# Kernel optimization log

Measured on AMD Instinct MI355X. Metric: run time of the kernel, lower is better.

The kernel has to match this reference:

```python
import jax, jax.numpy as jnp
import numpy as np

N = 100000      # nodes
E = 1600000     # directed edges (before self-loops)
F_IN, H1, H2 = 128, 64, 32


def setup_inputs() -> dict:
    key = jax.random.key(0)
    ks = jax.random.split(key, 8)
    x = jax.random.normal(ks[0], (N, F_IN), dtype=jnp.float32)
    edge_index = jax.random.randint(ks[1], (2, E), 0, N, dtype=jnp.int32)
    # GCNConv lin weights (no bias in lin; separate additive bias), glorot-ish scale
    W1 = jax.random.normal(ks[2], (F_IN, H1), dtype=jnp.float32) / np.sqrt(F_IN)
    b1 = jnp.zeros((H1,), dtype=jnp.float32)
    W2 = jax.random.normal(ks[3], (H1, H2), dtype=jnp.float32) / np.sqrt(H1)
    b2 = jnp.zeros((H2,), dtype=jnp.float32)
    Wfc = jax.random.normal(ks[4], (H2, 1), dtype=jnp.float32) / np.sqrt(H2)
    bfc = jnp.zeros((1,), dtype=jnp.float32)
    return {"x": x, "edge_index": edge_index, "W1": W1, "b1": b1,
            "W2": W2, "b2": b2, "Wfc": Wfc, "bfc": bfc}


def _gcn_norm(edge_index):
    # PyG GCNConv default: add self-loops, symmetric normalization D^-1/2 (A+I) D^-1/2
    loop = jnp.arange(N, dtype=edge_index.dtype)
    src = jnp.concatenate([edge_index[0], loop])
    dst = jnp.concatenate([edge_index[1], loop])
    deg = jax.ops.segment_sum(jnp.ones_like(dst, dtype=jnp.float32), dst, num_segments=N)
    dinv = jnp.where(deg > 0, jax.lax.rsqrt(deg), 0.0)
    norm = dinv[src] * dinv[dst]  # [E+N]
    return src, dst, norm


def _gcn_conv(x, W, b, src, dst, norm):
    h = x @ W                                 # project first (PyG order)
    msg = norm[:, None] * h[src]              # gather + scale
    agg = jax.ops.segment_sum(msg, dst, num_segments=N)  # scatter-add
    return agg + b


def reference(x, edge_index, W1, b1, W2, b2, Wfc, bfc):
    src, dst, norm = _gcn_norm(edge_index)
    h = jax.nn.relu(_gcn_conv(x, W1, b1, src, dst, norm))
    h = jax.nn.relu(_gcn_conv(h, W2, b2, src, dst, norm))
    return h @ Wfc + bfc
```

## Files before the change

### kernel.cpp

```cpp
#include <hip/hip_runtime.h>

#define N_NODES 100000
#define BSH 9
#define NBKT ((N_NODES + 511) >> BSH)
#define CH 7168
#define SLACK 10240

typedef unsigned int u32;
typedef unsigned short u16;
typedef unsigned char u8;
typedef __attribute__((ext_vector_type(8))) short s8v;
typedef __attribute__((ext_vector_type(4))) float f4v;

static __device__ __forceinline__ u16 f2bf(float f) {
    union { float f; u32 u; } c; c.f = f;
    u32 r = (c.u + 0x7fffu + ((c.u >> 16) & 1u)) >> 16;
    return (u16)r;
}
static __device__ __forceinline__ float bf2f_u(u16 h) {
    union { u32 u; float f; } c; c.u = ((u32)h) << 16;
    return c.f;
}
static __device__ __forceinline__ void acc2(u32 p, float& a, float& b) {
    union { u32 u; float f; } lo, hi;
    lo.u = p << 16;
    hi.u = p & 0xffff0000u;
    a += lo.f;
    b += hi.f;
}
static __device__ __forceinline__ void acc8(uint4 p, float* a) {
    acc2(p.x, a[0], a[1]); acc2(p.y, a[2], a[3]);
    acc2(p.z, a[4], a[5]); acc2(p.w, a[6], a[7]);
}


__global__ __launch_bounds__(256) void initcur_k(int* __restrict__ bcur) {
    bcur[threadIdx.x] = threadIdx.x * SLACK;
}

__global__ __launch_bounds__(256) void partition_k(const int* __restrict__ src,
        const int* __restrict__ dst, int* __restrict__ bcur,
        u32* __restrict__ bktBuf, int E, int TOT) {
    __shared__ int hist[256];
    __shared__ int lbase[256];
    __shared__ int gbase[256];
    __shared__ int ps[256];
    __shared__ u32 stage[CH];
    __shared__ u8 stageB[CH];
    int t = threadIdx.x;
    int base = blockIdx.x * CH;
    int cnt = min(CH, TOT - base);
    hist[t] = 0;
    __syncthreads();
    for (int i = t; i < cnt; i += 256) {
        int e = base + i;
        int d = (e < E) ? dst[e] : e - E;
        atomicAdd(&hist[d >> BSH], 1);
    }
    __syncthreads();
    ps[t] = hist[t];
    __syncthreads();
    for (int off = 1; off < 256; off <<= 1) {
        int val = ps[t];
        int add = (t >= off) ? ps[t - off] : 0;
        __syncthreads();
        ps[t] = val + add;
        __syncthreads();
    }
    lbase[t] = ps[t] - hist[t];
    gbase[t] = atomicAdd(&bcur[t], hist[t]);
    hist[t] = 0;
    __syncthreads();
    for (int i = t; i < cnt; i += 256) {
        int e = base + i;
        int s, d;
        if (e < E) { s = src[e]; d = dst[e]; }
        else       { s = d = e - E; }
        int b = d >> BSH;
        int lpos = lbase[b] + atomicAdd(&hist[b], 1);
        stage[lpos] = ((u32)(d & 511) << 17) | (u32)s;
        stageB[lpos] = (u8)b;
    }
    __syncthreads();
    for (int i = t; i < cnt; i += 256) {
        int b = stageB[i];
        bktBuf[gbase[b] + (i - lbase[b])] = stage[i];
    }
}

__global__ __launch_bounds__(256) void buildfill_k(const int* __restrict__ bcur,
        const u32* __restrict__ bktBuf, int* __restrict__ offsets,
        int* __restrict__ ends, float* __restrict__ dinv,
        int* __restrict__ srt_src) {
    __shared__ int hist[512];
    __shared__ int hscan[512];
    __shared__ int cur[512];
    __shared__ int ps[256];
    int t = threadIdx.x;
    int b = blockIdx.x;
    int v0 = b << BSH;
    int nv = min(512, N_NODES - v0);
    int base = b * SLACK;
    int cnt = bcur[b] - base;
    hist[t] = 0; hist[t + 256] = 0;
    cur[t] = 0;  cur[t + 256] = 0;
    __syncthreads();
    for (int i = t; i < cnt; i += 256)
        atomicAdd(&hist[bktBuf[base + i] >> 17], 1);
    __syncthreads();
    int a = hist[2 * t], bb = hist[2 * t + 1];
    int own = a + bb;
    ps[t] = own;
    __syncthreads();
    for (int off = 1; off < 256; off <<= 1) {
        int val = ps[t];
        int add = (t >= off) ? ps[t - off] : 0;
        __syncthreads();
        ps[t] = val + add;
        __syncthreads();
    }
    int excl2 = ps[t] - own;
    hscan[2 * t] = excl2;
    hscan[2 * t + 1] = excl2 + a;
    __syncthreads();
    for (int j = t; j < nv; j += 256) {
        int o = base + hscan[j];
        offsets[v0 + j] = o;
        ends[v0 + j] = o + hist[j];
        dinv[v0 + j] = rsqrtf((float)hist[j]);
    }
    for (int i = t; i < cnt; i += 256) {
        u32 it = bktBuf[base + i];
        int j = it >> 17;
        int pos = atomicAdd(&cur[j], 1);
        srt_src[base + hscan[j] + pos] = (int)(it & 0x1ffffu);
    }
}


static __device__ __forceinline__ void split8(const float* __restrict__ xp,
                                              s8v& hi, s8v& lo) {
    float4 v0 = *(const float4*)xp;
    float4 v1 = *(const float4*)(xp + 4);
    float xv[8] = {v0.x, v0.y, v0.z, v0.w, v1.x, v1.y, v1.z, v1.w};
#pragma unroll
    for (int j = 0; j < 8; ++j) {
        u16 h = f2bf(xv[j]);
        hi[j] = (short)h;
        lo[j] = (short)f2bf(xv[j] - bf2f_u(h));
    }
}

__global__ __launch_bounds__(256) void gemm1_k(const float* __restrict__ x,
                                               const float* __restrict__ W1,
                                               const float* __restrict__ dinv,
                                               u16* __restrict__ h1b) {
    __shared__ __attribute__((aligned(16))) short Bs[2][4][4][512];
    int t = threadIdx.x;
    for (int i = t; i < 128 * 64; i += 256) {
        int k = i >> 6, c = i & 63;
        float w = W1[i];
        u16 h = f2bf(w);
        u16 l = f2bf(w - bf2f_u(h));
        int ks = k >> 5, kg = (k >> 3) & 3, kk = k & 7;
        int ct = c >> 4, col = c & 15;
        int idx = (kg * 16 + col) * 8 + kk;
        Bs[0][ks][ct][idx] = (short)h;
        Bs[1][ks][ct][idx] = (short)l;
    }
    __syncthreads();

    int lane = t & 63;
    int rows0 = (blockIdx.x * 4 + (t >> 6)) * 32;
    if (rows0 >= N_NODES) return;

    f4v acc[2][4];
#pragma unroll
    for (int rt = 0; rt < 2; ++rt)
#pragma unroll
        for (int ct = 0; ct < 4; ++ct)
            acc[rt][ct] = (f4v){0.f, 0.f, 0.f, 0.f};

    int arow = lane & 15;
    int kgl = lane >> 4;
#pragma unroll
    for (int ks = 0; ks < 4; ++ks) {
        s8v bh[4], bl[4];
#pragma unroll
        for (int ct = 0; ct < 4; ++ct) {
            bh[ct] = *(const s8v*)&Bs[0][ks][ct][lane * 8];
            bl[ct] = *(const s8v*)&Bs[1][ks][ct][lane * 8];
        }
#pragma unroll
        for (int rt = 0; rt < 2; ++rt) {
            s8v ah, al;
            const float* xp = x + (size_t)(rows0 + rt * 16 + arow) * 128
                                + ks * 32 + kgl * 8;
            split8(xp, ah, al);
#pragma unroll
            for (int ct = 0; ct < 4; ++ct) {
                acc[rt][ct] = __builtin_amdgcn_mfma_f32_16x16x32_bf16(
                    ah, bh[ct], acc[rt][ct], 0, 0, 0);
                acc[rt][ct] = __builtin_amdgcn_mfma_f32_16x16x32_bf16(
                    ah, bl[ct], acc[rt][ct], 0, 0, 0);
                acc[rt][ct] = __builtin_amdgcn_mfma_f32_16x16x32_bf16(
                    al, bh[ct], acc[rt][ct], 0, 0, 0);
            }
        }
    }

#pragma unroll
    for (int rt = 0; rt < 2; ++rt) {
        int rbase = rows0 + rt * 16 + ((lane >> 4) << 2);
        float dv[4];
#pragma unroll
        for (int r = 0; r < 4; ++r) dv[r] = dinv[rbase + r];
#pragma unroll
        for (int ct = 0; ct < 4; ++ct) {
            int col = ct * 16 + (lane & 15);
#pragma unroll
            for (int r = 0; r < 4; ++r)
                h1b[(size_t)(rbase + r) * 64 + col] = f2bf(acc[rt][ct][r] * dv[r]);
        }
    }
}


__global__ __launch_bounds__(256) void layer2_k(const int* __restrict__ offsets,
        const int* __restrict__ ends, const int* __restrict__ srt_src,
        const float* __restrict__ dinv, const u16* __restrict__ h1b,
        const float* __restrict__ b1, const float* __restrict__ W2,
        u16* __restrict__ h2b) {
    __shared__ float W2s[64 * 32];
    __shared__ float b1s[64];
    for (int i = threadIdx.x; i < 64 * 32; i += 256) W2s[i] = W2[i];
    if (threadIdx.x < 64) b1s[threadIdx.x] = b1[threadIdx.x];
    __syncthreads();
    int lane = threadIdx.x & 63;
    int f = lane & 15, q = lane >> 4;
    int v0 = blockIdx.x * 8 + (threadIdx.x >> 6) * 2;
    int v1 = v0 + 1;
    int i0 = offsets[v0], e0 = ends[v0];
    int i1 = offsets[v1], e1 = ends[v1];
    const uint2* rows = (const uint2*)h1b;
    float a0 = 0.f, a1 = 0.f, a2 = 0.f, a3 = 0.f;
    float c0 = 0.f, c1 = 0.f, c2 = 0.f, c3 = 0.f;
    while (i0 + 8 <= e0 && i1 + 8 <= e1) {
        int sA = srt_src[i0 + q];
        int sB = srt_src[i0 + 4 + q];
        int sC = srt_src[i1 + q];
        int sD = srt_src[i1 + 4 + q];
        uint2 pA = rows[sA * 16 + f];
        uint2 pB = rows[sB * 16 + f];
        uint2 pC = rows[sC * 16 + f];
        uint2 pD = rows[sD * 16 + f];
        acc2(pA.x, a0, a1); acc2(pA.y, a2, a3);
        acc2(pB.x, a0, a1); acc2(pB.y, a2, a3);
        acc2(pC.x, c0, c1); acc2(pC.y, c2, c3);
        acc2(pD.x, c0, c1); acc2(pD.y, c2, c3);
        i0 += 8; i1 += 8;
    }
    for (; i0 + 8 <= e0; i0 += 8) {
        int sA = srt_src[i0 + q], sB = srt_src[i0 + 4 + q];
        uint2 pA = rows[sA * 16 + f], pB = rows[sB * 16 + f];
        acc2(pA.x, a0, a1); acc2(pA.y, a2, a3);
        acc2(pB.x, a0, a1); acc2(pB.y, a2, a3);
    }
    for (; i0 < e0; i0 += 4) {
        int j = i0 + q;
        if (j < e0) {
            int s = srt_src[j];
            uint2 p = rows[s * 16 + f];
            acc2(p.x, a0, a1); acc2(p.y, a2, a3);
        }
    }
    for (; i1 + 8 <= e1; i1 += 8) {
        int sA = srt_src[i1 + q], sB = srt_src[i1 + 4 + q];
        uint2 pA = rows[sA * 16 + f], pB = rows[sB * 16 + f];
        acc2(pA.x, c0, c1); acc2(pA.y, c2, c3);
        acc2(pB.x, c0, c1); acc2(pB.y, c2, c3);
    }
    for (; i1 < e1; i1 += 4) {
        int j = i1 + q;
        if (j < e1) {
            int s = srt_src[j];
            uint2 p = rows[s * 16 + f];
            acc2(p.x, c0, c1); acc2(p.y, c2, c3);
        }
    }
    a0 += __shfl_xor(a0, 16, 64); a0 += __shfl_xor(a0, 32, 64);
    a1 += __shfl_xor(a1, 16, 64); a1 += __shfl_xor(a1, 32, 64);
    a2 += __shfl_xor(a2, 16, 64); a2 += __shfl_xor(a2, 32, 64);
    a3 += __shfl_xor(a3, 16, 64); a3 += __shfl_xor(a3, 32, 64);
    c0 += __shfl_xor(c0, 16, 64); c0 += __shfl_xor(c0, 32, 64);
    c1 += __shfl_xor(c1, 16, 64); c1 += __shfl_xor(c1, 32, 64);
    c2 += __shfl_xor(c2, 16, 64); c2 += __shfl_xor(c2, 32, 64);
    c3 += __shfl_xor(c3, 16, 64); c3 += __shfl_xor(c3, 32, 64);
    bool lo = (lane < 32);
    float dv = lo ? dinv[v0] : dinv[v1];
    float t0 = lo ? a0 : c0;
    float t1 = lo ? a1 : c1;
    float t2 = lo ? a2 : c2;
    float t3 = lo ? a3 : c3;
    float r0 = fmaxf(fmaf(dv, t0, b1s[4 * f + 0]), 0.f);
    float r1 = fmaxf(fmaf(dv, t1, b1s[4 * f + 1]), 0.f);
    float r2 = fmaxf(fmaf(dv, t2, b1s[4 * f + 2]), 0.f);
    float r3 = fmaxf(fmaf(dv, t3, b1s[4 * f + 3]), 0.f);
    int c = lane & 31;
    float o = 0.f;
#pragma unroll
    for (int j2 = 0; j2 < 16; ++j2) {
        float R0 = __shfl(r0, j2, 16);
        float R1 = __shfl(r1, j2, 16);
        float R2 = __shfl(r2, j2, 16);
        float R3 = __shfl(r3, j2, 16);
        o = fmaf(R0, W2s[(4 * j2 + 0) * 32 + c], o);
        o = fmaf(R1, W2s[(4 * j2 + 1) * 32 + c], o);
        o = fmaf(R2, W2s[(4 * j2 + 2) * 32 + c], o);
        o = fmaf(R3, W2s[(4 * j2 + 3) * 32 + c], o);
    }
    int vst = lo ? v0 : v1;
    h2b[vst * 32 + c] = f2bf(dv * o);
}


#define GATH3(ii, A, B, C, D) { \
    int s_ = srt_src[(ii) + oc]; \
    uint2 p_ = rows[s_ * 8 + f]; \
    acc2(p_.x, A, B); acc2(p_.y, C, D); }

__global__ __launch_bounds__(256) void layer3_k(const int* __restrict__ offsets,
        const int* __restrict__ ends, const int* __restrict__ srt_src,
        const float* __restrict__ dinv, const u16* __restrict__ h2b,
        const float* __restrict__ b2, const float* __restrict__ Wfc,
        const float* __restrict__ bfc, float* __restrict__ out) {
    int lane = threadIdx.x & 63;
    int f = lane & 7, oc = lane >> 3;
    int vb = blockIdx.x * 16 + (threadIdx.x >> 6) * 4;
    int i0 = offsets[vb],     e0 = ends[vb];
    int i1 = offsets[vb + 1], e1 = ends[vb + 1];
    int i2 = offsets[vb + 2], e2 = ends[vb + 2];
    int i3 = offsets[vb + 3], e3 = ends[vb + 3];
    const uint2* rows = (const uint2*)h2b;
    float A0=0.f,A1=0.f,A2=0.f,A3=0.f, B0=0.f,B1=0.f,B2=0.f,B3=0.f;
    float C0=0.f,C1=0.f,C2=0.f,C3=0.f, D0=0.f,D1=0.f,D2=0.f,D3=0.f;
    while (i0 + 8 <= e0 && i1 + 8 <= e1 && i2 + 8 <= e2 && i3 + 8 <= e3) {
        GATH3(i0, A0, A1, A2, A3);
        GATH3(i1, B0, B1, B2, B3);
        GATH3(i2, C0, C1, C2, C3);
        GATH3(i3, D0, D1, D2, D3);
        i0 += 8; i1 += 8; i2 += 8; i3 += 8;
    }
    while (i0 + 8 <= e0) { GATH3(i0, A0, A1, A2, A3); i0 += 8; }
    if (i0 + oc < e0)    { GATH3(i0, A0, A1, A2, A3); }
    while (i1 + 8 <= e1) { GATH3(i1, B0, B1, B2, B3); i1 += 8; }
    if (i1 + oc < e1)    { GATH3(i1, B0, B1, B2, B3); }
    while (i2 + 8 <= e2) { GATH3(i2, C0, C1, C2, C3); i2 += 8; }
    if (i2 + oc < e2)    { GATH3(i2, C0, C1, C2, C3); }
    while (i3 + 8 <= e3) { GATH3(i3, D0, D1, D2, D3); i3 += 8; }
    if (i3 + oc < e3)    { GATH3(i3, D0, D1, D2, D3); }
#define RED3(X) X += __shfl_xor(X, 8, 64); X += __shfl_xor(X, 16, 64); X += __shfl_xor(X, 32, 64)
    RED3(A0); RED3(A1); RED3(A2); RED3(A3);
    RED3(B0); RED3(B1); RED3(B2); RED3(B3);
    RED3(C0); RED3(C1); RED3(C2); RED3(C3);
    RED3(D0); RED3(D1); RED3(D2); RED3(D3);
    float w0 = Wfc[4 * f + 0], w1 = Wfc[4 * f + 1];
    float w2 = Wfc[4 * f + 2], w3 = Wfc[4 * f + 3];
    float g0 = b2[4 * f + 0], g1 = b2[4 * f + 1];
    float g2 = b2[4 * f + 2], g3 = b2[4 * f + 3];
    float dv0 = dinv[vb], dv1 = dinv[vb + 1], dv2 = dinv[vb + 2], dv3 = dinv[vb + 3];
    float p0 = fmaxf(fmaf(dv0, A0, g0), 0.f) * w0 + fmaxf(fmaf(dv0, A1, g1), 0.f) * w1
             + fmaxf(fmaf(dv0, A2, g2), 0.f) * w2 + fmaxf(fmaf(dv0, A3, g3), 0.f) * w3;
    float p1 = fmaxf(fmaf(dv1, B0, g0), 0.f) * w0 + fmaxf(fmaf(dv1, B1, g1), 0.f) * w1
             + fmaxf(fmaf(dv1, B2, g2), 0.f) * w2 + fmaxf(fmaf(dv1, B3, g3), 0.f) * w3;
    float p2 = fmaxf(fmaf(dv2, C0, g0), 0.f) * w0 + fmaxf(fmaf(dv2, C1, g1), 0.f) * w1
             + fmaxf(fmaf(dv2, C2, g2), 0.f) * w2 + fmaxf(fmaf(dv2, C3, g3), 0.f) * w3;
    float p3 = fmaxf(fmaf(dv3, D0, g0), 0.f) * w0 + fmaxf(fmaf(dv3, D1, g1), 0.f) * w1
             + fmaxf(fmaf(dv3, D2, g2), 0.f) * w2 + fmaxf(fmaf(dv3, D3, g3), 0.f) * w3;
#define REDP(X) X += __shfl_xor(X, 1, 64); X += __shfl_xor(X, 2, 64); X += __shfl_xor(X, 4, 64)
    REDP(p0); REDP(p1); REDP(p2); REDP(p3);
    if (lane == 0) {
        float bb = bfc[0];
        out[vb + 0] = p0 + bb;
        out[vb + 1] = p1 + bb;
        out[vb + 2] = p2 + bb;
        out[vb + 3] = p3 + bb;
    }
}


extern "C" void kernel_launch(void* const* d_in, const int* in_sizes, int n_in,
                              void* d_out, int out_size, void* d_ws, size_t ws_size,
                              hipStream_t stream) {
    const float* x   = (const float*)d_in[0];
    const int*   ei  = (const int*)d_in[1];
    const float* W1  = (const float*)d_in[2];
    const float* b1  = (const float*)d_in[3];
    const float* W2  = (const float*)d_in[4];
    const float* b2  = (const float*)d_in[5];
    const float* Wfc = (const float*)d_in[6];
    const float* bfc = (const float*)d_in[7];
    float* out = (float*)d_out;

    const int E = in_sizes[1] / 2;
    const int TOT = E + N_NODES;
    const int* src = ei;
    const int* dst = ei + E;

    int*   bcur    = (int*)d_ws;
    int*   offsets = bcur + 256;
    int*   ends    = offsets + N_NODES;
    int*   srt_src = ends + N_NODES;
    u32*   bktBuf  = (u32*)(srt_src + NBKT * SLACK);
    float* dinv    = (float*)(bktBuf + NBKT * SLACK);
    u16*   h1b     = (u16*)(dinv + N_NODES);
    u16*   h2b     = h1b + (size_t)N_NODES * 64;

    const int NCH = (TOT + CH - 1) / CH;

    initcur_k<<<1, 256, 0, stream>>>(bcur);
    partition_k<<<NCH, 256, 0, stream>>>(src, dst, bcur, bktBuf, E, TOT);
    buildfill_k<<<NBKT, 256, 0, stream>>>(bcur, bktBuf, offsets, ends, dinv,
                                          srt_src);

    const int GB1 = (N_NODES / 32 + 3) / 4;
    gemm1_k<<<GB1, 256, 0, stream>>>(x, W1, dinv, h1b);

    layer2_k<<<N_NODES / 8, 256, 0, stream>>>(offsets, ends, srt_src, dinv, h1b,
                                              b1, W2, h2b);
    layer3_k<<<N_NODES / 16, 256, 0, stream>>>(offsets, ends, srt_src, dinv, h2b,
                                               b2, Wfc, bfc, out);
}
```

Measured before the change: 187.7 us.

## Widen gathers to 16-byte rows and walk contiguous CSR span across owned nodes

Layers 2 and 3 now load 8 bf16 features per lane with uint4 gathers instead of 4 via uint2. Each wave walks the contiguous edge range covering all the nodes it owns, so a group that straddles a node boundary is split by the per-edge index rather than handled by a separate tail loop per node. The intent is fewer, wider memory transactions and fewer partially filled tail iterations. In exchange it adds more accumulator registers, longer shuffle reductions, and relies on the nodes' edge ranges being adjacent (ends[v0] == offsets[v1]); acc8 is assumed to be defined in the unseen part of the file.

```diff
diff --git a/kernel.cpp b/kernel.cpp
--- a/kernel.cpp
+++ b/kernel.cpp
@@ -237,97 +237,76 @@
     if (threadIdx.x < 64) b1s[threadIdx.x] = b1[threadIdx.x];
     __syncthreads();
     int lane = threadIdx.x & 63;
-    int f = lane & 15, q = lane >> 4;
+    int f = lane & 7, q = lane >> 3;
     int v0 = blockIdx.x * 8 + (threadIdx.x >> 6) * 2;
     int v1 = v0 + 1;
-    int i0 = offsets[v0], e0 = ends[v0];
-    int i1 = offsets[v1], e1 = ends[v1];
-    const uint2* rows = (const uint2*)h1b;
-    float a0 = 0.f, a1 = 0.f, a2 = 0.f, a3 = 0.f;
-    float c0 = 0.f, c1 = 0.f, c2 = 0.f, c3 = 0.f;
-    while (i0 + 8 <= e0 && i1 + 8 <= e1) {
-        int sA = srt_src[i0 + q];
-        int sB = srt_src[i0 + 4 + q];
-        int sC = srt_src[i1 + q];
-        int sD = srt_src[i1 + 4 + q];
-        uint2 pA = rows[sA * 16 + f];
-        uint2 pB = rows[sB * 16 + f];
-        uint2 pC = rows[sC * 16 + f];
-        uint2 pD = rows[sD * 16 + f];
-        acc2(pA.x, a0, a1); acc2(pA.y, a2, a3);
-        acc2(pB.x, a0, a1); acc2(pB.y, a2, a3);
-        acc2(pC.x, c0, c1); acc2(pC.y, c2, c3);
-        acc2(pD.x, c0, c1); acc2(pD.y, c2, c3);
-        i0 += 8; i1 += 8;
-    }
-    for (; i0 + 8 <= e0; i0 += 8) {
-        int sA = srt_src[i0 + q], sB = srt_src[i0 + 4 + q];
-        uint2 pA = rows[sA * 16 + f], pB = rows[sB * 16 + f];
-        acc2(pA.x, a0, a1); acc2(pA.y, a2, a3);
-        acc2(pB.x, a0, a1); acc2(pB.y, a2, a3);
-    }
-    for (; i0 < e0; i0 += 4) {
-        int j = i0 + q;
-        if (j < e0) {
-            int s = srt_src[j];
-            uint2 p = rows[s * 16 + f];
-            acc2(p.x, a0, a1); acc2(p.y, a2, a3);
+    int beg = offsets[v0], m = ends[v0], end = ends[v1];
+    const uint4* rows = (const uint4*)h1b;
+    float a[8] = {0.f,0.f,0.f,0.f,0.f,0.f,0.f,0.f};
+    float c[8] = {0.f,0.f,0.f,0.f,0.f,0.f,0.f,0.f};
+    int i = beg;
+    for (; i + 16 <= m; i += 16) {
+        int sA = srt_src[i + q], sB = srt_src[i + 8 + q];
+        uint4 pA = rows[(size_t)sA * 8 + f];
+        uint4 pB = rows[(size_t)sB * 8 + f];
+        acc8(pA, a); acc8(pB, a);
+    }
+    if (i + 8 <= m) {
+        int s = srt_src[i + q];
+        acc8(rows[(size_t)s * 8 + f], a);
+        i += 8;
+    }
+    if (i < m) {
+        int j = i + q;
+        if (j < end) {
+            uint4 p = rows[(size_t)srt_src[j] * 8 + f];
+            if (j < m) acc8(p, a); else acc8(p, c);
         }
-    }
-    for (; i1 + 8 <= e1; i1 += 8) {
-        int sA = srt_src[i1 + q], sB = srt_src[i1 + 4 + q];
-        uint2 pA = rows[sA * 16 + f], pB = rows[sB * 16 + f];
-        acc2(pA.x, c0, c1); acc2(pA.y, c2, c3);
-        acc2(pB.x, c0, c1); acc2(pB.y, c2, c3);
-    }
-    for (; i1 < e1; i1 += 4) {
-        int j = i1 + q;
-        if (j < e1) {
-            int s = srt_src[j];
-            uint2 p = rows[s * 16 + f];
-            acc2(p.x, c0, c1); acc2(p.y, c2, c3);
-        }
-    }
-    a0 += __shfl_xor(a0, 16, 64); a0 += __shfl_xor(a0, 32, 64);
-    a1 += __shfl_xor(a1, 16, 64); a1 += __shfl_xor(a1, 32, 64);
-    a2 += __shfl_xor(a2, 16, 64); a2 += __shfl_xor(a2, 32, 64);
-    a3 += __shfl_xor(a3, 16, 64); a3 += __shfl_xor(a3, 32, 64);
-    c0 += __shfl_xor(c0, 16, 64); c0 += __shfl_xor(c0, 32, 64);
-    c1 += __shfl_xor(c1, 16, 64); c1 += __shfl_xor(c1, 32, 64);
-    c2 += __shfl_xor(c2, 16, 64); c2 += __shfl_xor(c2, 32, 64);
-    c3 += __shfl_xor(c3, 16, 64); c3 += __shfl_xor(c3, 32, 64);
+        i += 8;
+    }
+    for (; i + 16 <= end; i += 16) {
+        int sA = srt_src[i + q], sB = srt_src[i + 8 + q];
+        uint4 pA = rows[(size_t)sA * 8 + f];
+        uint4 pB = rows[(size_t)sB * 8 + f];
+        acc8(pA, c); acc8(pB, c);
+    }
+    if (i + 8 <= end) {
+        int s = srt_src[i + q];
+        acc8(rows[(size_t)s * 8 + f], c);
+        i += 8;
+    }
+    if (i + q < end) {
+        acc8(rows[(size_t)srt_src[i + q] * 8 + f], c);
+    }
+#pragma unroll
+    for (int j = 0; j < 8; ++j) {
+        a[j] += __shfl_xor(a[j], 8, 64);
+        a[j] += __shfl_xor(a[j], 16, 64);
+        a[j] += __shfl_xor(a[j], 32, 64);
+        c[j] += __shfl_xor(c[j], 8, 64);
+        c[j] += __shfl_xor(c[j], 16, 64);
+        c[j] += __shfl_xor(c[j], 32, 64);
+    }
     bool lo = (lane < 32);
     float dv = lo ? dinv[v0] : dinv[v1];
-    float t0 = lo ? a0 : c0;
-    float t1 = lo ? a1 : c1;
-    float t2 = lo ? a2 : c2;
-    float t3 = lo ? a3 : c3;
-    float r0 = fmaxf(fmaf(dv, t0, b1s[4 * f + 0]), 0.f);
-    float r1 = fmaxf(fmaf(dv, t1, b1s[4 * f + 1]), 0.f);
-    float r2 = fmaxf(fmaf(dv, t2, b1s[4 * f + 2]), 0.f);
-    float r3 = fmaxf(fmaf(dv, t3, b1s[4 * f + 3]), 0.f);
-    int c = lane & 31;
+    float r[8];
+#pragma unroll
+    for (int j = 0; j < 8; ++j) {
+        float tv = lo ? a[j] : c[j];
+        r[j] = fmaxf(fmaf(dv, tv, b1s[8 * f + j]), 0.f);
+    }
+    int cc = lane & 31;
     float o = 0.f;
 #pragma unroll
-    for (int j2 = 0; j2 < 16; ++j2) {
-        float R0 = __shfl(r0, j2, 16);
-        float R1 = __shfl(r1, j2, 16);
-        float R2 = __shfl(r2, j2, 16);
-        float R3 = __shfl(r3, j2, 16);
-        o = fmaf(R0, W2s[(4 * j2 + 0) * 32 + c], o);
-        o = fmaf(R1, W2s[(4 * j2 + 1) * 32 + c], o);
-        o = fmaf(R2, W2s[(4 * j2 + 2) * 32 + c], o);
-        o = fmaf(R3, W2s[(4 * j2 + 3) * 32 + c], o);
+    for (int g = 0; g < 8; ++g) {
+#pragma unroll
+        for (int j = 0; j < 8; ++j)
+            o = fmaf(__shfl(r[j], g, 8), W2s[(8 * g + j) * 32 + cc], o);
     }
     int vst = lo ? v0 : v1;
-    h2b[vst * 32 + c] = f2bf(dv * o);
-}
-
-
-#define GATH3(ii, A, B, C, D) { \
-    int s_ = srt_src[(ii) + oc]; \
-    uint2 p_ = rows[s_ * 8 + f]; \
-    acc2(p_.x, A, B); acc2(p_.y, C, D); }
+    h2b[(size_t)vst * 32 + cc] = f2bf(dv * o);
+}
+
 
 __global__ __launch_bounds__(256) void layer3_k(const int* __restrict__ offsets,
         const int* __restrict__ ends, const int* __restrict__ srt_src,
@@ -335,56 +314,83 @@
         const float* __restrict__ b2, const float* __restrict__ Wfc,
         const float* __restrict__ bfc, float* __restrict__ out) {
     int lane = threadIdx.x & 63;
-    int f = lane & 7, oc = lane >> 3;
+    int f = lane & 3, q = lane >> 2;
     int vb = blockIdx.x * 16 + (threadIdx.x >> 6) * 4;
-    int i0 = offsets[vb],     e0 = ends[vb];
-    int i1 = offsets[vb + 1], e1 = ends[vb + 1];
-    int i2 = offsets[vb + 2], e2 = ends[vb + 2];
-    int i3 = offsets[vb + 3], e3 = ends[vb + 3];
-    const uint2* rows = (const uint2*)h2b;
-    float A0=0.f,A1=0.f,A2=0.f,A3=0.f, B0=0.f,B1=0.f,B2=0.f,B3=0.f;
-    float C0=0.f,C1=0.f,C2=0.f,C3=0.f, D0=0.f,D1=0.f,D2=0.f,D3=0.f;
-    while (i0 + 8 <= e0 && i1 + 8 <= e1 && i2 + 8 <= e2 && i3 + 8 <= e3) {
-        GATH3(i0, A0, A1, A2, A3);
-        GATH3(i1, B0, B1, B2, B3);
-        GATH3(i2, C0, C1, C2, C3);
-        GATH3(i3, D0, D1, D2, D3);
-        i0 += 8; i1 += 8; i2 += 8; i3 += 8;
-    }
-    while (i0 + 8 <= e0) { GATH3(i0, A0, A1, A2, A3); i0 += 8; }
-    if (i0 + oc < e0)    { GATH3(i0, A0, A1, A2, A3); }
-    while (i1 + 8 <= e1) { GATH3(i1, B0, B1, B2, B3); i1 += 8; }
-    if (i1 + oc < e1)    { GATH3(i1, B0, B1, B2, B3); }
-    while (i2 + 8 <= e2) { GATH3(i2, C0, C1, C2, C3); i2 += 8; }
-    if (i2 + oc < e2)    { GATH3(i2, C0, C1, C2, C3); }
-    while (i3 + 8 <= e3) { GATH3(i3, D0, D1, D2, D3); i3 += 8; }
-    if (i3 + oc < e3)    { GATH3(i3, D0, D1, D2, D3); }
-#define RED3(X) X += __shfl_xor(X, 8, 64); X += __shfl_xor(X, 16, 64); X += __shfl_xor(X, 32, 64)
-    RED3(A0); RED3(A1); RED3(A2); RED3(A3);
-    RED3(B0); RED3(B1); RED3(B2); RED3(B3);
-    RED3(C0); RED3(C1); RED3(C2); RED3(C3);
-    RED3(D0); RED3(D1); RED3(D2); RED3(D3);
-    float w0 = Wfc[4 * f + 0], w1 = Wfc[4 * f + 1];
-    float w2 = Wfc[4 * f + 2], w3 = Wfc[4 * f + 3];
-    float g0 = b2[4 * f + 0], g1 = b2[4 * f + 1];
-    float g2 = b2[4 * f + 2], g3 = b2[4 * f + 3];
+    int beg = offsets[vb];
+    int m1 = ends[vb], m2 = ends[vb + 1], m3 = ends[vb + 2], end = ends[vb + 3];
+    const uint4* rows = (const uint4*)h2b;
+    float A[8] = {0.f,0.f,0.f,0.f,0.f,0.f,0.f,0.f};
+    float B[8] = {0.f,0.f,0.f,0.f,0.f,0.f,0.f,0.f};
+    float C[8] = {0.f,0.f,0.f,0.f,0.f,0.f,0.f,0.f};
+    float D[8] = {0.f,0.f,0.f,0.f,0.f,0.f,0.f,0.f};
+    int i = beg;
+#define STRADDLE(MK) \
+    if (i < MK) { \
+        int j = i + q; \
+        if (j < end) { \
+            uint4 p = rows[(size_t)srt_src[j] * 4 + f]; \
+            if (j < m1) acc8(p, A); \
+            else if (j < m2) acc8(p, B); \
+            else if (j < m3) acc8(p, C); \
+            else acc8(p, D); \
+        } \
+        i += 16; \
+    }
+    for (; i + 16 <= m1; i += 16) {
+        int s = srt_src[i + q];
+        acc8(rows[(size_t)s * 4 + f], A);
+    }
+    STRADDLE(m1)
+    for (; i + 16 <= m2; i += 16) {
+        int s = srt_src[i + q];
+        acc8(rows[(size_t)s * 4 + f], B);
+    }
+    STRADDLE(m2)
+    for (; i + 16 <= m3; i += 16) {
+        int s = srt_src[i + q];
+        acc8(rows[(size_t)s * 4 + f], C);
+    }
+    STRADDLE(m3)
+    for (; i + 16 <= end; i += 16) {
+        int s = srt_src[i + q];
+        acc8(rows[(size_t)s * 4 + f], D);
+    }
+    if (i + q < end) {
+        acc8(rows[(size_t)srt_src[i + q] * 4 + f], D);
+    }
+#undef STRADDLE
+#pragma unroll
+    for (int j = 0; j < 8; ++j) {
+        A[j] += __shfl_xor(A[j], 4, 64);  A[j] += __shfl_xor(A[j], 8, 64);
+        A[j] += __shfl_xor(A[j], 16, 64); A[j] += __shfl_xor(A[j], 32, 64);
+        B[j] += __shfl_xor(B[j], 4, 64);  B[j] += __shfl_xor(B[j], 8, 64);
+        B[j] += __shfl_xor(B[j], 16, 64); B[j] += __shfl_xor(B[j], 32, 64);
+        C[j] += __shfl_xor(C[j], 4, 64);  C[j] += __shfl_xor(C[j], 8, 64);
+        C[j] += __shfl_xor(C[j], 16, 64); C[j] += __shfl_xor(C[j], 32, 64);
+        D[j] += __shfl_xor(D[j], 4, 64);  D[j] += __shfl_xor(D[j], 8, 64);
+        D[j] += __shfl_xor(D[j], 16, 64); D[j] += __shfl_xor(D[j], 32, 64);
+    }
     float dv0 = dinv[vb], dv1 = dinv[vb + 1], dv2 = dinv[vb + 2], dv3 = dinv[vb + 3];
-    float p0 = fmaxf(fmaf(dv0, A0, g0), 0.f) * w0 + fmaxf(fmaf(dv0, A1, g1), 0.f) * w1
-             + fmaxf(fmaf(dv0, A2, g2), 0.f) * w2 + fmaxf(fmaf(dv0, A3, g3), 0.f) * w3;
-    float p1 = fmaxf(fmaf(dv1, B0, g0), 0.f) * w0 + fmaxf(fmaf(dv1, B1, g1), 0.f) * w1
-             + fmaxf(fmaf(dv1, B2, g2), 0.f) * w2 + fmaxf(fmaf(dv1, B3, g3), 0.f) * w3;
-    float p2 = fmaxf(fmaf(dv2, C0, g0), 0.f) * w0 + fmaxf(fmaf(dv2, C1, g1), 0.f) * w1
-             + fmaxf(fmaf(dv2, C2, g2), 0.f) * w2 + fmaxf(fmaf(dv2, C3, g3), 0.f) * w3;
-    float p3 = fmaxf(fmaf(dv3, D0, g0), 0.f) * w0 + fmaxf(fmaf(dv3, D1, g1), 0.f) * w1
-             + fmaxf(fmaf(dv3, D2, g2), 0.f) * w2 + fmaxf(fmaf(dv3, D3, g3), 0.f) * w3;
-#define REDP(X) X += __shfl_xor(X, 1, 64); X += __shfl_xor(X, 2, 64); X += __shfl_xor(X, 4, 64)
-    REDP(p0); REDP(p1); REDP(p2); REDP(p3);
+    float pr0 = 0.f, pr1 = 0.f, pr2 = 0.f, pr3 = 0.f;
+#pragma unroll
+    for (int j = 0; j < 8; ++j) {
+        int k = 8 * f + j;
+        float w = Wfc[k], g = b2[k];
+        pr0 += fmaxf(fmaf(dv0, A[j], g), 0.f) * w;
+        pr1 += fmaxf(fmaf(dv1, B[j], g), 0.f) * w;
+        pr2 += fmaxf(fmaf(dv2, C[j], g), 0.f) * w;
+        pr3 += fmaxf(fmaf(dv3, D[j], g), 0.f) * w;
+    }
+    pr0 += __shfl_xor(pr0, 1, 64); pr0 += __shfl_xor(pr0, 2, 64);
+    pr1 += __shfl_xor(pr1, 1, 64); pr1 += __shfl_xor(pr1, 2, 64);
+    pr2 += __shfl_xor(pr2, 1, 64); pr2 += __shfl_xor(pr2, 2, 64);
+    pr3 += __shfl_xor(pr3, 1, 64); pr3 += __shfl_xor(pr3, 2, 64);
     if (lane == 0) {
         float bb = bfc[0];
-        out[vb + 0] = p0 + bb;
-        out[vb + 1] = p1 + bb;
-        out[vb + 2] = p2 + bb;
-        out[vb + 3] = p3 + bb;
+        out[vb + 0] = pr0 + bb;
+        out[vb + 1] = pr1 + bb;
+        out[vb + 2] = pr2 + bb;
+        out[vb + 3] = pr3 + bb;
     }
 }
 
```

Measured after the change: 204.3 us. 8.8% more time.
